# Optimization experiments

Hardware: AMD Instinct MI355X
Metric: run time of the kernel (lower is better)

## Reference

```python
import jax, jax.numpy as jnp
import numpy as np

NI, ND, NH = 64, 64, 4
NB, NLOC, NNEI = 4, 2048, 64


def setup_inputs() -> dict:
    key = jax.random.key(0)
    ks = jax.random.split(key, 7)
    g1 = jax.random.normal(ks[0], (NB, NLOC, NI), dtype=jnp.float32)
    gg1 = jax.random.normal(ks[1], (NB, NLOC, NNEI, NI), dtype=jnp.float32)
    nlist_mask = jax.random.randint(ks[2], (NB, NLOC, NNEI), 0, 2).astype(bool)
    # torch Linear weight (out, in); store transposed for x @ W
    Wq = jax.random.normal(ks[3], (NI, ND * NH), dtype=jnp.float32) * (1.0 / np.sqrt(NI))
    Wkv = jax.random.normal(ks[4], (NI, (ND + NI) * NH), dtype=jnp.float32) * (1.0 / np.sqrt(NI))
    Wh = jax.random.normal(ks[5], (NI * NH, NI), dtype=jnp.float32) * (1.0 / np.sqrt(NI * NH))
    bh = jax.random.normal(ks[6], (NI,), dtype=jnp.float32) * 0.01
    return {"g1": g1, "gg1": gg1, "nlist_mask": nlist_mask,
            "Wq": Wq, "Wkv": Wkv, "Wh": Wh, "bh": bh}


def reference(g1, gg1, nlist_mask, Wq, Wkv, Wh, bh):
    nb, nloc, nnei = nlist_mask.shape
    ni, nd, nh = NI, ND, NH
    # q: (nb, nloc, nh, nd)
    q = (g1 @ Wq).reshape(nb, nloc, nd, nh).transpose(0, 1, 3, 2)
    # kv: (nb, nloc, nnei, nd, 2*nh) -> (nb, nloc, 2*nh, nnei, nd); valid since ni == nd
    kv = (gg1 @ Wkv).reshape(nb, nloc, nnei, nd, 2 * nh).transpose(0, 1, 4, 2, 3)
    k = kv[:, :, :nh]          # (nb, nloc, nh, nnei, nd)
    v = kv[:, :, nh:2 * nh]    # (nb, nloc, nh, nnei, nd)
    attnw = jnp.einsum('blhd,blhjd->blhj', q, k) / np.sqrt(nd).astype(np.float32)
    m = nlist_mask[:, :, None, :]  # (nb, nloc, 1, nnei)
    attnw = jnp.where(m, attnw, -jnp.inf)
    attnw = jax.nn.softmax(attnw, axis=-1)
    attnw = jnp.where(m, attnw, 0.0)
    ret = jnp.einsum('blhj,blhjd->blhd', attnw, v).reshape(nb, nloc, nh * ni)
    return ret @ Wh + bh
```

## Files before the change

kernel.cpp:

```cpp
#include <hip/hip_runtime.h>
#include <hip/hip_fp16.h>
#include <math.h>

#define NATOM 8192

namespace {

typedef _Float16 half8 __attribute__((ext_vector_type(8)));
typedef _Float16 half2t __attribute__((ext_vector_type(2)));
typedef float f32x4 __attribute__((ext_vector_type(4)));

constexpr int VB_STRIDE = 260;

__global__ void pack_weights(const float* __restrict__ Wkv,
                             const float* __restrict__ Wq,
                             const float* __restrict__ Wh,
                             _Float16* __restrict__ out) {
  int tid = blockIdx.x * 256 + threadIdx.x;
  if (tid < 32768) {
    int i = tid >> 9, c = tid & 511;
    int ks = i >> 5, jj = i & 7, lq = (i >> 3) & 3;
    int ct = c >> 4, lr = c & 15;
    int l = lq * 16 + lr;
    out[(((ct * 2 + ks) * 64) + l) * 8 + jj] = (_Float16)Wkv[i * 512 + c];
  } else if (tid < 49152) {
    int idx = tid - 32768;
    int i = idx >> 8, c = idx & 255;
    out[32768 + c * 64 + i] = (_Float16)Wq[i * 256 + c];
  } else {
    int idx = tid - 49152;
    int k = idx >> 6, c = idx & 63;
    out[49152 + c * 256 + k] = (_Float16)Wh[k * 64 + c];
  }
}

__device__ __forceinline__ float dot8(half8 a, half8 b, float acc) {
  acc = __builtin_amdgcn_fdot2((half2t){a[0], a[1]}, (half2t){b[0], b[1]}, acc, false);
  acc = __builtin_amdgcn_fdot2((half2t){a[2], a[3]}, (half2t){b[2], b[3]}, acc, false);
  acc = __builtin_amdgcn_fdot2((half2t){a[4], a[5]}, (half2t){b[4], b[5]}, acc, false);
  acc = __builtin_amdgcn_fdot2((half2t){a[6], a[7]}, (half2t){b[6], b[7]}, acc, false);
  return acc;
}

__global__ __launch_bounds__(256, 4)
void local_atten_kernel(const float* __restrict__ g1,
                        const float* __restrict__ gg1,
                        const int* __restrict__ mask,
                        const _Float16* __restrict__ wpack,
                        const float* __restrict__ bh,
                        float* __restrict__ out) {
  __shared__ __align__(16) __half vraw[64 * VB_STRIDE];
  __shared__ __align__(16) __half g1h[64];
  __shared__ __align__(16) unsigned char blob[3072];
  __shared__ __align__(8) __half aws2[64][4];
  __shared__ __align__(16) __half rets[256];

  float* qs = reinterpret_cast<float*>(blob);
  __half (*sred)[4][64] = reinterpret_cast<__half(*)[4][64]>(blob + 1024);
  __half (*redbuf2)[64][4] = reinterpret_cast<__half(*)[64][4]>(blob);
  float (*redbuf)[64] = reinterpret_cast<float(*)[64]>(blob + 2048);

  const _Float16* wkvp = wpack;
  const _Float16* wqp  = wpack + 32768;
  const _Float16* whp  = wpack + 49152;

  const int t = threadIdx.x;
  const int lane = t & 63;
  const int wave = t >> 6;
  const int lq = lane >> 4;
  const int lr = lane & 15;
  const int atom = blockIdx.x;

  __half* gs = vraw;
  auto vbuf = reinterpret_cast<__half(*)[VB_STRIDE]>(vraw);

  const int mreg = mask[(size_t)atom * 64 + lane];
  const float bhv = bh[lane];
  if (t < 64) g1h[t] = __float2half(g1[(size_t)atom * 64 + t]);

  {
    const float4* src = reinterpret_cast<const float4*>(gg1 + (size_t)atom * 4096);
#pragma unroll
    for (int r = 0; r < 4; ++r) {
      int idx4 = t + 256 * r;
      int j = idx4 >> 4;
      int i4 = (idx4 & 15) << 2;
      float4 v = src[idx4];
      __half2 h01 = __floats2half2_rn(v.x, v.y);
      __half2 h23 = __floats2half2_rn(v.z, v.w);
      int g = i4 >> 3;
      int addr = j * 64 + ((g ^ (j & 7)) << 3) + (i4 & 7);
      union { __half2 h[2]; uint2 u; } pk;
      pk.h[0] = h01; pk.h[1] = h23;
      *reinterpret_cast<uint2*>(&gs[addr]) = pk.u;
    }
  }
  __syncthreads();

  half8 bfrag[4][2];
#pragma unroll
  for (int jt = 0; jt < 4; ++jt) {
#pragma unroll
    for (int ks = 0; ks < 2; ++ks) {
      int j = jt * 16 + lr;
      int g = ks * 4 + lq;
      bfrag[jt][ks] =
          *reinterpret_cast<const half8*>(&gs[j * 64 + ((g ^ (j & 7)) << 3)]);
    }
  }

  const half8* ap_base = reinterpret_cast<const half8*>(wkvp);
  half8 a0 = ap_base[(wave * 4) * 128 + lane];
  half8 a1 = ap_base[(wave * 4) * 128 + 64 + lane];

  {
    float qacc = 0.f;
    const half8* wrow = reinterpret_cast<const half8*>(wqp + t * 64);
    const half8* grow = reinterpret_cast<const half8*>(&g1h[0]);
#pragma unroll
    for (int ks = 0; ks < 8; ++ks) qacc = dot8(wrow[ks], grow[ks], qacc);
    qs[t] = qacc;
  }
  __syncthreads();

  float sacc[4][4];
#pragma unroll
  for (int jt = 0; jt < 4; ++jt)
#pragma unroll
    for (int h = 0; h < 4; ++h) sacc[jt][h] = 0.f;

  const bool isv = (lq & 1);
#pragma unroll
  for (int it = 0; it < 8; ++it) {
    const int ct = ((it >> 2) << 4) + wave * 4 + (it & 3);
    const int d = ct * 2 + (lq >> 1);

    half8 na0 = a0, na1 = a1;
    if (it < 7) {
      const int nit = it + 1;
      const int nct = ((nit >> 2) << 4) + wave * 4 + (nit & 3);
      na0 = ap_base[nct * 128 + lane];
      na1 = ap_base[nct * 128 + 64 + lane];
    }

    f32x4 accs[4];
#pragma unroll
    for (int jt = 0; jt < 4; ++jt) {
      f32x4 acc = {0.f, 0.f, 0.f, 0.f};
      acc = __builtin_amdgcn_mfma_f32_16x16x32_f16(a0, bfrag[jt][0], acc, 0, 0, 0);
      acc = __builtin_amdgcn_mfma_f32_16x16x32_f16(a1, bfrag[jt][1], acc, 0, 0, 0);
      accs[jt] = acc;
    }

    if (isv) {
#pragma unroll
      for (int jt = 0; jt < 4; ++jt) {
        int j = jt * 16 + lr;
        __half2 h01 = __floats2half2_rn(accs[jt][0], accs[jt][1]);
        __half2 h23 = __floats2half2_rn(accs[jt][2], accs[jt][3]);
        union { __half2 h[2]; uint2 u; } pk;
        pk.h[0] = h01; pk.h[1] = h23;
        *reinterpret_cast<uint2*>(&vbuf[j][d * 4]) = pk.u;
      }
    } else {
      float4 q4 = *reinterpret_cast<const float4*>(&qs[d * 4]);
#pragma unroll
      for (int jt = 0; jt < 4; ++jt) {
        sacc[jt][0] = fmaf(accs[jt][0], q4.x, sacc[jt][0]);
        sacc[jt][1] = fmaf(accs[jt][1], q4.y, sacc[jt][1]);
        sacc[jt][2] = fmaf(accs[jt][2], q4.z, sacc[jt][2]);
        sacc[jt][3] = fmaf(accs[jt][3], q4.w, sacc[jt][3]);
      }
    }
    a0 = na0; a1 = na1;
  }

#pragma unroll
  for (int jt = 0; jt < 4; ++jt)
#pragma unroll
    for (int h = 0; h < 4; ++h)
      sacc[jt][h] += __shfl_xor(sacc[jt][h], 32);
  if (lq == 0) {
#pragma unroll
    for (int h = 0; h < 4; ++h)
#pragma unroll
      for (int jt = 0; jt < 4; ++jt)
        sred[wave][h][jt * 16 + lr] = __float2half(sacc[jt][h]);
  }
  __syncthreads();

  half8 wh_frag[8];
  {
    const half8* wrow = reinterpret_cast<const half8*>(whp + lane * 256 + wave * 64);
#pragma unroll
    for (int ks = 0; ks < 8; ++ks) wh_frag[ks] = wrow[ks];
  }

  {
    float s = __half2float(sred[0][wave][lane]) + __half2float(sred[1][wave][lane]) +
              __half2float(sred[2][wave][lane]) + __half2float(sred[3][wave][lane]);
    s *= 0.125f;
    s = mreg ? s : -INFINITY;
    float mx = s;
#pragma unroll
    for (int off = 32; off > 0; off >>= 1) mx = fmaxf(mx, __shfl_xor(mx, off));
    float pe = mreg ? __expf(s - mx) : 0.f;
    float sum = pe;
#pragma unroll
    for (int off = 32; off > 0; off >>= 1) sum += __shfl_xor(sum, off);
    float aw = (sum > 0.f) ? (pe / sum) : 0.f;
    aws2[lane][wave] = __float2half(aw);
  }
  __syncthreads();

  {
    __half2 o01 = __float2half2_rn(0.f), o23 = __float2half2_rn(0.f);
#pragma unroll
    for (int jj = 0; jj < 16; ++jj) {
      int j = wave * 16 + jj;
      union { uint2 u; __half2 h[2]; } aw, vv;
      aw.u = *reinterpret_cast<const uint2*>(&aws2[j][0]);
      vv.u = *reinterpret_cast<const uint2*>(&vbuf[j][lane * 4]);
      o01 = __hfma2(aw.h[0], vv.h[0], o01);
      o23 = __hfma2(aw.h[1], vv.h[1], o23);
    }
    union { uint2 u; __half2 h[2]; } pk;
    pk.h[0] = o01; pk.h[1] = o23;
    *reinterpret_cast<uint2*>(&redbuf2[wave][lane][0]) = pk.u;
  }
  __syncthreads();

  {
    float r = 0.f;
#pragma unroll
    for (int jq = 0; jq < 4; ++jq) r += __half2float(redbuf2[jq][lane][wave]);
    rets[wave * 64 + lane] = __float2half(r);
  }

  {
    float part = 0.f;
    const half8* rrow = reinterpret_cast<const half8*>(&rets[wave * 64]);
#pragma unroll
    for (int ks = 0; ks < 8; ++ks) part = dot8(wh_frag[ks], rrow[ks], part);
    redbuf[wave][lane] = part;
  }
  __syncthreads();
  if (t < 64)
    out[(size_t)atom * 64 + t] =
        redbuf[0][t] + redbuf[1][t] + redbuf[2][t] + redbuf[3][t] + bhv;
}

}

extern "C" void kernel_launch(void* const* d_in, const int* in_sizes, int n_in,
                              void* d_out, int out_size, void* d_ws, size_t ws_size,
                              hipStream_t stream) {
  const float* g1   = (const float*)d_in[0];
  const float* gg1  = (const float*)d_in[1];
  const int*   mask = (const int*)d_in[2];
  const float* Wq   = (const float*)d_in[3];
  const float* Wkv  = (const float*)d_in[4];
  const float* Wh   = (const float*)d_in[5];
  const float* bh   = (const float*)d_in[6];
  float* out = (float*)d_out;
  (void)in_sizes; (void)n_in; (void)ws_size; (void)out_size;

  _Float16* wpack = (_Float16*)d_ws;
  pack_weights<<<256, 256, 0, stream>>>(Wkv, Wq, Wh, wpack);
  local_atten_kernel<<<NATOM, 256, 0, stream>>>(g1, gg1, mask, wpack, bh, out);
}
```

Measured before the change: 269.2 us.

## Split K and V projections into separate phases, drop V buffer, raise occupancy

The Wkv packing is reordered so the K and V output tiles are separated. The kernel now computes the K projection and scores first, then recomputes MFMA tiles for V after the softmax and contracts them directly with the attention weights in registers, using shuffles to reduce. This removes the large shared-memory V buffer and the bfrag and wh_frag register arrays, and the launch bounds ask for 8 blocks per CU instead of 4. B fragments are now reloaded from LDS each iteration and the weight-load prefetching is gone, which adds LDS traffic and extra shuffle reductions in exchange for lower LDS use and register pressure.

After: 427.0 us. +58.6%, slower.

```diff
diff --git a/kernel.cpp b/kernel.cpp
--- a/kernel.cpp
+++ b/kernel.cpp
@@ -9,8 +9,6 @@
 typedef _Float16 half8 __attribute__((ext_vector_type(8)));
 typedef _Float16 half2t __attribute__((ext_vector_type(2)));
 typedef float f32x4 __attribute__((ext_vector_type(4)));
-
-constexpr int VB_STRIDE = 260;
 
 __global__ void pack_weights(const float* __restrict__ Wkv,
                              const float* __restrict__ Wq,
@@ -19,10 +17,12 @@
   int tid = blockIdx.x * 256 + threadIdx.x;
   if (tid < 32768) {
     int i = tid >> 9, c = tid & 511;
-    int ks = i >> 5, jj = i & 7, lq = (i >> 3) & 3;
-    int ct = c >> 4, lr = c & 15;
-    int l = lq * 16 + lr;
-    out[(((ct * 2 + ks) * 64) + l) * 8 + jj] = (_Float16)Wkv[i * 512 + c];
+    int ks = i >> 5, jj = i & 7, lqk = (i >> 3) & 3;
+    int d = c >> 3, e = c & 7, isv = e >> 2, h = e & 3;
+    int T = isv * 16 + (d >> 2);
+    int m = ((d & 3) << 2) | h;
+    int l = lqk * 16 + m;
+    out[(((T * 2 + ks) * 64) + l) * 8 + jj] = (_Float16)Wkv[i * 512 + c];
   } else if (tid < 49152) {
     int idx = tid - 32768;
     int i = idx >> 8, c = idx & 255;
@@ -42,14 +42,14 @@
   return acc;
 }
 
-__global__ __launch_bounds__(256, 4)
+__global__ __launch_bounds__(256, 8)
 void local_atten_kernel(const float* __restrict__ g1,
                         const float* __restrict__ gg1,
                         const int* __restrict__ mask,
                         const _Float16* __restrict__ wpack,
                         const float* __restrict__ bh,
                         float* __restrict__ out) {
-  __shared__ __align__(16) __half vraw[64 * VB_STRIDE];
+  __shared__ __align__(16) __half gs[64 * 64];
   __shared__ __align__(16) __half g1h[64];
   __shared__ __align__(16) unsigned char blob[3072];
   __shared__ __align__(8) __half aws2[64][4];
@@ -57,8 +57,7 @@
 
   float* qs = reinterpret_cast<float*>(blob);
   __half (*sred)[4][64] = reinterpret_cast<__half(*)[4][64]>(blob + 1024);
-  __half (*redbuf2)[64][4] = reinterpret_cast<__half(*)[64][4]>(blob);
-  float (*redbuf)[64] = reinterpret_cast<float(*)[64]>(blob + 2048);
+  float (*redbuf)[64] = reinterpret_cast<float(*)[64]>(blob);
 
   const _Float16* wkvp = wpack;
   const _Float16* wqp  = wpack + 32768;
@@ -70,9 +69,6 @@
   const int lq = lane >> 4;
   const int lr = lane & 15;
   const int atom = blockIdx.x;
-
-  __half* gs = vraw;
-  auto vbuf = reinterpret_cast<__half(*)[VB_STRIDE]>(vraw);
 
   const int mreg = mask[(size_t)atom * 64 + lane];
   const float bhv = bh[lane];
@@ -95,24 +91,11 @@
       *reinterpret_cast<uint2*>(&gs[addr]) = pk.u;
     }
   }
-  __syncthreads();
-
-  half8 bfrag[4][2];
-#pragma unroll
-  for (int jt = 0; jt < 4; ++jt) {
-#pragma unroll
-    for (int ks = 0; ks < 2; ++ks) {
-      int j = jt * 16 + lr;
-      int g = ks * 4 + lq;
-      bfrag[jt][ks] =
-          *reinterpret_cast<const half8*>(&gs[j * 64 + ((g ^ (j & 7)) << 3)]);
-    }
-  }
-
-  const half8* ap_base = reinterpret_cast<const half8*>(wkvp);
-  half8 a0 = ap_base[(wave * 4) * 128 + lane];
-  half8 a1 = ap_base[(wave * 4) * 128 + 64 + lane];
-
+
+  const __half* bp0 = &gs[lr * 64 + ((lq ^ (lr & 7)) << 3)];
+  const __half* bp1 = &gs[lr * 64 + (((4 + lq) ^ (lr & 7)) << 3)];
+
+  __syncthreads();
   {
     float qacc = 0.f;
     const half8* wrow = reinterpret_cast<const half8*>(wqp + t * 64);
@@ -123,63 +106,42 @@
   }
   __syncthreads();
 
+  const half8* ap_base = reinterpret_cast<const half8*>(wkvp);
+
   float sacc[4][4];
 #pragma unroll
   for (int jt = 0; jt < 4; ++jt)
 #pragma unroll
     for (int h = 0; h < 4; ++h) sacc[jt][h] = 0.f;
 
-  const bool isv = (lq & 1);
-#pragma unroll
-  for (int it = 0; it < 8; ++it) {
-    const int ct = ((it >> 2) << 4) + wave * 4 + (it & 3);
-    const int d = ct * 2 + (lq >> 1);
-
-    half8 na0 = a0, na1 = a1;
-    if (it < 7) {
-      const int nit = it + 1;
-      const int nct = ((nit >> 2) << 4) + wave * 4 + (nit & 3);
-      na0 = ap_base[nct * 128 + lane];
-      na1 = ap_base[nct * 128 + 64 + lane];
-    }
-
-    f32x4 accs[4];
+#pragma unroll
+  for (int it = 0; it < 4; ++it) {
+    const int T = wave * 4 + it;
+    half8 a0 = ap_base[T * 128 + lane];
+    half8 a1 = ap_base[T * 128 + 64 + lane];
+    const int d = T * 4 + lq;
+    float4 q4 = *reinterpret_cast<const float4*>(&qs[d * 4]);
 #pragma unroll
     for (int jt = 0; jt < 4; ++jt) {
+      half8 b0 = *reinterpret_cast<const half8*>(bp0 + jt * 1024);
+      half8 b1 = *reinterpret_cast<const half8*>(bp1 + jt * 1024);
       f32x4 acc = {0.f, 0.f, 0.f, 0.f};
-      acc = __builtin_amdgcn_mfma_f32_16x16x32_f16(a0, bfrag[jt][0], acc, 0, 0, 0);
-      acc = __builtin_amdgcn_mfma_f32_16x16x32_f16(a1, bfrag[jt][1], acc, 0, 0, 0);
-      accs[jt] = acc;
-    }
-
-    if (isv) {
-#pragma unroll
-      for (int jt = 0; jt < 4; ++jt) {
-        int j = jt * 16 + lr;
-        __half2 h01 = __floats2half2_rn(accs[jt][0], accs[jt][1]);
-        __half2 h23 = __floats2half2_rn(accs[jt][2], accs[jt][3]);
-        union { __half2 h[2]; uint2 u; } pk;
-        pk.h[0] = h01; pk.h[1] = h23;
-        *reinterpret_cast<uint2*>(&vbuf[j][d * 4]) = pk.u;
-      }
-    } else {
-      float4 q4 = *reinterpret_cast<const float4*>(&qs[d * 4]);
-#pragma unroll
-      for (int jt = 0; jt < 4; ++jt) {
-        sacc[jt][0] = fmaf(accs[jt][0], q4.x, sacc[jt][0]);
-        sacc[jt][1] = fmaf(accs[jt][1], q4.y, sacc[jt][1]);
-        sacc[jt][2] = fmaf(accs[jt][2], q4.z, sacc[jt][2]);
-        sacc[jt][3] = fmaf(accs[jt][3], q4.w, sacc[jt][3]);
-      }
-    }
-    a0 = na0; a1 = na1;
+      acc = __builtin_amdgcn_mfma_f32_16x16x32_f16(a0, b0, acc, 0, 0, 0);
+      acc = __builtin_amdgcn_mfma_f32_16x16x32_f16(a1, b1, acc, 0, 0, 0);
+      sacc[jt][0] = fmaf(acc[0], q4.x, sacc[jt][0]);
+      sacc[jt][1] = fmaf(acc[1], q4.y, sacc[jt][1]);
+      sacc[jt][2] = fmaf(acc[2], q4.z, sacc[jt][2]);
+      sacc[jt][3] = fmaf(acc[3], q4.w, sacc[jt][3]);
+    }
   }
 
 #pragma unroll
   for (int jt = 0; jt < 4; ++jt)
 #pragma unroll
-    for (int h = 0; h < 4; ++h)
+    for (int h = 0; h < 4; ++h) {
+      sacc[jt][h] += __shfl_xor(sacc[jt][h], 16);
       sacc[jt][h] += __shfl_xor(sacc[jt][h], 32);
+    }
   if (lq == 0) {
 #pragma unroll
     for (int h = 0; h < 4; ++h)
@@ -188,13 +150,6 @@
         sred[wave][h][jt * 16 + lr] = __float2half(sacc[jt][h]);
   }
   __syncthreads();
-
-  half8 wh_frag[8];
-  {
-    const half8* wrow = reinterpret_cast<const half8*>(whp + lane * 256 + wave * 64);
-#pragma unroll
-    for (int ks = 0; ks < 8; ++ks) wh_frag[ks] = wrow[ks];
-  }
 
   {
     float s = __half2float(sred[0][wave][lane]) + __half2float(sred[1][wave][lane]) +
@@ -213,35 +168,55 @@
   }
   __syncthreads();
 
-  {
-    __half2 o01 = __float2half2_rn(0.f), o23 = __float2half2_rn(0.f);
-#pragma unroll
-    for (int jj = 0; jj < 16; ++jj) {
-      int j = wave * 16 + jj;
-      union { uint2 u; __half2 h[2]; } aw, vv;
-      aw.u = *reinterpret_cast<const uint2*>(&aws2[j][0]);
-      vv.u = *reinterpret_cast<const uint2*>(&vbuf[j][lane * 4]);
-      o01 = __hfma2(aw.h[0], vv.h[0], o01);
-      o23 = __hfma2(aw.h[1], vv.h[1], o23);
-    }
-    union { uint2 u; __half2 h[2]; } pk;
-    pk.h[0] = o01; pk.h[1] = o23;
-    *reinterpret_cast<uint2*>(&redbuf2[wave][lane][0]) = pk.u;
-  }
-  __syncthreads();
-
-  {
-    float r = 0.f;
-#pragma unroll
-    for (int jq = 0; jq < 4; ++jq) r += __half2float(redbuf2[jq][lane][wave]);
-    rets[wave * 64 + lane] = __float2half(r);
-  }
+  float awf[4][4];
+#pragma unroll
+  for (int jt = 0; jt < 4; ++jt) {
+    union { uint2 u; __half2 h[2]; } awu;
+    awu.u = *reinterpret_cast<const uint2*>(&aws2[jt * 16 + lr][0]);
+    float2 f01 = __half22float2(awu.h[0]);
+    float2 f23 = __half22float2(awu.h[1]);
+    awf[jt][0] = f01.x; awf[jt][1] = f01.y; awf[jt][2] = f23.x; awf[jt][3] = f23.y;
+  }
+
+#pragma unroll
+  for (int it = 0; it < 4; ++it) {
+    const int T = 16 + wave * 4 + it;
+    half8 a0 = ap_base[T * 128 + lane];
+    half8 a1 = ap_base[T * 128 + 64 + lane];
+    float part[4] = {0.f, 0.f, 0.f, 0.f};
+#pragma unroll
+    for (int jt = 0; jt < 4; ++jt) {
+      half8 b0 = *reinterpret_cast<const half8*>(bp0 + jt * 1024);
+      half8 b1 = *reinterpret_cast<const half8*>(bp1 + jt * 1024);
+      f32x4 acc = {0.f, 0.f, 0.f, 0.f};
+      acc = __builtin_amdgcn_mfma_f32_16x16x32_f16(a0, b0, acc, 0, 0, 0);
+      acc = __builtin_amdgcn_mfma_f32_16x16x32_f16(a1, b1, acc, 0, 0, 0);
+      part[0] = fmaf(acc[0], awf[jt][0], part[0]);
+      part[1] = fmaf(acc[1], awf[jt][1], part[1]);
+      part[2] = fmaf(acc[2], awf[jt][2], part[2]);
+      part[3] = fmaf(acc[3], awf[jt][3], part[3]);
+    }
+#pragma unroll
+    for (int r = 0; r < 4; ++r) {
+      part[r] += __shfl_xor(part[r], 1);
+      part[r] += __shfl_xor(part[r], 2);
+      part[r] += __shfl_xor(part[r], 4);
+      part[r] += __shfl_xor(part[r], 8);
+    }
+    if (lr == 0) {
+      const int d = (T - 16) * 4 + lq;
+#pragma unroll
+      for (int r = 0; r < 4; ++r) rets[r * 64 + d] = __float2half(part[r]);
+    }
+  }
+  __syncthreads();
 
   {
     float part = 0.f;
+    const half8* wrow = reinterpret_cast<const half8*>(whp + lane * 256 + wave * 64);
     const half8* rrow = reinterpret_cast<const half8*>(&rets[wave * 64]);
 #pragma unroll
-    for (int ks = 0; ks < 8; ++ks) part = dot8(wh_frag[ks], rrow[ks], part);
+    for (int ks = 0; ks < 8; ++ks) part = dot8(wrow[ks], rrow[ks], part);
     redbuf[wave][lane] = part;
   }
   __syncthreads();
```
